# Performance work log

Hardware: AMD Instinct MI355X
Metric: run time of the kernel (lower is better)

## Reference

```python
import jax, jax.numpy as jnp
import numpy as np

N = 50000      # nodes
E = 1600000    # edges (before self loops)
IN = 128
OUT = 128
H = 4
HD = OUT // H  # head dim = 32


def setup_inputs() -> dict:
    key = jax.random.key(0)
    k1, k2, k3, k4, k5 = jax.random.split(key, 5)
    x = jax.random.normal(k1, (N, IN), dtype=jnp.float32)
    edge_index = jax.random.randint(k2, (2, E), 0, N, dtype=jnp.int64)
    # xavier-uniform-ish scales
    W = jax.random.normal(k3, (OUT, IN), dtype=jnp.float32) * (1.0 / np.sqrt(IN))
    att_src = jax.random.normal(k4, (1, H, HD), dtype=jnp.float32) * 0.1
    att_dst = jax.random.normal(k5, (1, H, HD), dtype=jnp.float32) * 0.1
    return {"x": x, "edge_index": edge_index, "W": W, "att_src": att_src, "att_dst": att_dst}


def reference(x, edge_index, W, att_src, att_dst):
    n = x.shape[0]
    # add self loops (tg.utils.add_self_loops appends [i, i] edges)
    loops = jnp.arange(n, dtype=edge_index.dtype)
    ei = jnp.concatenate([edge_index, jnp.stack([loops, loops])], axis=1)
    src, dst = ei[0], ei[1]

    # linear projection, split into heads: [n, H, HD]
    h = (x @ W.T).reshape(n, H, HD)

    # per-node attention logits per head: [n, H]
    a_src = jnp.sum(h * att_src, axis=-1)
    a_dst = jnp.sum(h * att_dst, axis=-1)

    # per-edge attention score: gather + leaky_relu
    alpha = a_src[src] + a_dst[dst]                      # [Etot, H]
    alpha = jax.nn.leaky_relu(alpha, negative_slope=0.2)

    # segment softmax grouped by destination node (numerically stable)
    m = jax.ops.segment_max(alpha, dst, num_segments=n)  # [n, H]
    e = jnp.exp(alpha - m[dst])
    s = jax.ops.segment_sum(e, dst, num_segments=n)      # [n, H]
    e = e / s[dst]                                       # [Etot, H]

    # weighted scatter-add aggregation; f_additive adds 1 to the weights
    msg = h[src] * (e[:, :, None] + 1.0)                 # [Etot, H, HD]
    out = jax.ops.segment_sum(msg, dst, num_segments=n)  # [n, H, HD]
    return out.reshape(n, -1)
```

## Files before the change

kernel.cpp:

```cpp
#include <hip/hip_runtime.h>

#define N_NODES 50000
#define E_EDGES 1600000
#define ETOT    (E_EDGES + N_NODES)
#define DIN  128
#define DOUT 128
#define NH   4
#define HD   32

typedef unsigned short ushort_t;
typedef unsigned int uint_t;
typedef __attribute__((ext_vector_type(8))) short bfrag;
typedef __attribute__((ext_vector_type(4))) float ffrag;

__device__ __forceinline__ ushort_t f2bf(float f) {
  uint_t u = __float_as_uint(f);
  u += 0x7fffu + ((u >> 16) & 1u);
  return (ushort_t)(u >> 16);
}
__device__ __forceinline__ float bf_lo(uint_t u) {
  return __uint_as_float(u << 16);
}
__device__ __forceinline__ float bf_hi(uint_t u) {
  return __uint_as_float(u & 0xffff0000u);
}

#define BSZ   64
#define NBUCK ((N_NODES + BSZ - 1) / BSZ)
#define CAP   2560
#define EPB_A 4096
#define NBLK_A ((ETOT + EPB_A - 1) / EPB_A)
#define NCHUNK 13

__global__ __launch_bounds__(256, 4) void fused_binA_gemm_kernel(
    const int* __restrict__ ei, int* __restrict__ gcur,
    uint_t* __restrict__ ebuf,
    const float* __restrict__ x, const float* __restrict__ W,
    const float* __restrict__ att_src, const float* __restrict__ att_dst,
    ushort_t* __restrict__ hb, float* __restrict__ a_src,
    float* __restrict__ a_dst) {
  __shared__ int hist[NBUCK];
  __shared__ int base[NBUCK];
  __shared__ ushort_t Ws[DIN * DOUT];
  const int tid = threadIdx.x;

  if (blockIdx.x < NBLK_A) {
    const int e0 = blockIdx.x * EPB_A;
    const int e1 = min(e0 + EPB_A, ETOT);
    for (int i = tid; i < NBUCK; i += 256) hist[i] = 0;
    __syncthreads();
    for (int e = e0 + tid; e < e1; e += 256) {
      int di = (e < E_EDGES) ? ei[E_EDGES + e] : (e - E_EDGES);
      atomicAdd(&hist[di >> 6], 1);
    }
    __syncthreads();
    for (int i = tid; i < NBUCK; i += 256) {
      int c = hist[i];
      base[i] = (c > 0) ? (i * CAP + atomicAdd(&gcur[i], c)) : 0;
      hist[i] = 0;
    }
    __syncthreads();
    for (int e = e0 + tid; e < e1; e += 256) {
      int si, di;
      if (e < E_EDGES) { si = ei[e]; di = ei[E_EDGES + e]; }
      else             { si = e - E_EDGES; di = si; }
      int b = di >> 6;
      int pos = base[b] + atomicAdd(&hist[b], 1);
      if (pos < (b + 1) * CAP)
        ebuf[pos] = ((uint_t)(di & 63) << 24) | (uint_t)si;
    }
    return;
  }

  const int gb = blockIdx.x - NBLK_A;
  for (int u = tid; u < 2048; u += 256) {
    int row = u >> 4;
    float4 w0 = *(const float4*)&W[u * 8];
    float4 w1 = *(const float4*)&W[u * 8 + 4];
    uint4 pk;
    pk.x = (uint_t)f2bf(w0.x) | ((uint_t)f2bf(w0.y) << 16);
    pk.y = (uint_t)f2bf(w0.z) | ((uint_t)f2bf(w0.w) << 16);
    pk.z = (uint_t)f2bf(w1.x) | ((uint_t)f2bf(w1.y) << 16);
    pk.w = (uint_t)f2bf(w1.z) | ((uint_t)f2bf(w1.w) << 16);
    *(uint4*)&Ws[(u ^ (row & 7)) * 8] = pk;
  }
  __syncthreads();

  const int wv = tid >> 6, l = tid & 63;
  const int lr = l & 15, lg = l >> 4;
  const int nbase = gb * 64 + wv * 16;
  int na = nbase + lr;
  if (na >= N_NODES) na = N_NODES - 1;
  const float* xrow = x + (size_t)na * DIN;

  ffrag acc[8];
#pragma unroll
  for (int oc = 0; oc < 8; oc++) acc[oc] = (ffrag){0.f, 0.f, 0.f, 0.f};

#pragma unroll
  for (int kt = 0; kt < 4; kt++) {
    float4 x0 = *(const float4*)&xrow[kt * 32 + lg * 8];
    float4 x1 = *(const float4*)&xrow[kt * 32 + lg * 8 + 4];
    bfrag a;
    a[0] = (short)f2bf(x0.x); a[1] = (short)f2bf(x0.y);
    a[2] = (short)f2bf(x0.z); a[3] = (short)f2bf(x0.w);
    a[4] = (short)f2bf(x1.x); a[5] = (short)f2bf(x1.y);
    a[6] = (short)f2bf(x1.z); a[7] = (short)f2bf(x1.w);
#pragma unroll
    for (int oc = 0; oc < 8; oc++) {
      const int u = ((oc * 16 + lr) << 4) + kt * 4 + lg;
      const bfrag b = *(const bfrag*)&Ws[(u ^ (lr & 7)) * 8];
      acc[oc] = __builtin_amdgcn_mfma_f32_16x16x32_bf16(a, b, acc[oc], 0, 0, 0);
    }
  }

#pragma unroll
  for (int oc = 0; oc < 8; oc++) {
#pragma unroll
    for (int j = 0; j < 4; j++) {
      int n = nbase + lg * 4 + j;
      if (n < N_NODES)
        hb[((size_t)n << 7) + oc * 16 + lr] = f2bf(acc[oc][j]);
    }
  }

  float asv[8], adv[8];
#pragma unroll
  for (int oc = 0; oc < 8; oc++) {
    asv[oc] = att_src[oc * 16 + lr];
    adv[oc] = att_dst[oc * 16 + lr];
  }
#pragma unroll
  for (int j = 0; j < 4; j++) {
    float ps[4] = {0.f, 0.f, 0.f, 0.f};
    float pd[4] = {0.f, 0.f, 0.f, 0.f};
#pragma unroll
    for (int oc = 0; oc < 8; oc++) {
      ps[oc >> 1] = fmaf(acc[oc][j], asv[oc], ps[oc >> 1]);
      pd[oc >> 1] = fmaf(acc[oc][j], adv[oc], pd[oc >> 1]);
    }
#pragma unroll
    for (int off = 1; off < 16; off <<= 1) {
#pragma unroll
      for (int hd = 0; hd < 4; hd++) {
        ps[hd] += __shfl_xor(ps[hd], off);
        pd[hd] += __shfl_xor(pd[hd], off);
      }
    }
    int n = nbase + lg * 4 + j;
    if (n < N_NODES && lr < 4) {
      float vs = lr == 0 ? ps[0] : lr == 1 ? ps[1] : lr == 2 ? ps[2] : ps[3];
      float vd = lr == 0 ? pd[0] : lr == 1 ? pd[1] : lr == 2 ? pd[2] : pd[3];
      a_src[n * NH + lr] = vs;
      a_dst[n * NH + lr] = vd;
    }
  }
}

__global__ __launch_bounds__(256) void binB_kernel(
    const uint_t* __restrict__ ebuf, const int* __restrict__ gcur,
    int* __restrict__ rs, int* __restrict__ re, int* __restrict__ col) {
  __shared__ int cnt[BSZ * NCHUNK];
  __shared__ int roff[BSZ * NCHUNK];
  const int b = blockIdx.x;
  const int tid = threadIdx.x;
  const int n0 = b << 6;
  const int nn = min(BSZ, N_NODES - n0);
  const int s0 = b * CAP;
  const int s1 = s0 + min(gcur[b], CAP);
  for (int k = tid; k < BSZ * NCHUNK; k += 256) cnt[k] = 0;
  __syncthreads();
  for (int i = s0 + tid; i < s1; i += 256) {
    uint_t p = ebuf[i];
    int key = (int)(p >> 24) * NCHUNK + (int)((p & 0xFFFFFFu) >> 12);
    atomicAdd(&cnt[key], 1);
  }
  __syncthreads();
  if (tid < BSZ) {
    int pref[NCHUNK];
    int tot = 0;
#pragma unroll
    for (int k = 0; k < NCHUNK; k++) { pref[k] = tot; tot += cnt[tid * NCHUNK + k]; }
    int xx = tot;
#pragma unroll
    for (int off = 1; off < 64; off <<= 1) {
      int y = __shfl_up(xx, off, 64);
      if (tid >= off) xx += y;
    }
    const int nodebase = xx - tot;
#pragma unroll
    for (int k = 0; k < NCHUNK; k++) roff[tid * NCHUNK + k] = nodebase + pref[k];
    if (tid < nn) {
      rs[n0 + tid] = s0 + nodebase;
      re[n0 + tid] = s0 + nodebase + tot;
    }
  }
  __syncthreads();
  for (int k = tid; k < BSZ * NCHUNK; k += 256) cnt[k] = 0;
  __syncthreads();
  for (int i = s0 + tid; i < s1; i += 256) {
    uint_t p = ebuf[i];
    int si = (int)(p & 0xFFFFFFu);
    int key = (int)(p >> 24) * NCHUNK + (si >> 12);
    int pos = atomicAdd(&cnt[key], 1);
    int q = s0 + roff[key] + pos;
    if (q >= 0 && q < NBUCK * CAP) col[q] = si;
  }
}

#define NPB 16
#define CH  16

__global__ __launch_bounds__(256, 8) void agg_kernel(
    const int* __restrict__ col, const int* __restrict__ rs,
    const int* __restrict__ re, const ushort_t* __restrict__ hb,
    const float* __restrict__ a_src, const float* __restrict__ a_dst,
    float* __restrict__ out) {
  __shared__ float w_lds[NPB][CH][NH];
  __shared__ int   si_lds[NPB][CH];
  const int tid  = threadIdx.x;
  const int slot = tid >> 4;
  const int t    = tid & 15;
  const int node = blockIdx.x * NPB + slot;
  const int start = rs[node];
  const int deg   = re[node] - start;
  const float4 ad = *(const float4*)(a_dst + (size_t)node * NH);

  const int head = t >> 2;
  const int c8 = t << 3;
  const ushort_t* hc = hb + c8;
  float s = 0.f;
  float a0 = 0.f, a1 = 0.f, a2 = 0.f, a3 = 0.f;
  float a4 = 0.f, a5 = 0.f, a6 = 0.f, a7 = 0.f;
  float b0 = 0.f, b1 = 0.f, b2 = 0.f, b3 = 0.f;
  float b4 = 0.f, b5 = 0.f, b6 = 0.f, b7 = 0.f;

  for (int base_e = 0; base_e < deg; base_e += CH) {
    int nch = deg - base_e;
    if (nch > CH) nch = CH;
    if (t < nch) {
      int si = col[start + base_e + t];
      si = si < N_NODES ? si : 0;
      si_lds[slot][t] = si;
      float4 as = *(const float4*)(a_src + (size_t)si * NH);
      float v0 = as.x + ad.x; v0 = v0 > 0.f ? v0 : 0.2f * v0;
      float v1 = as.y + ad.y; v1 = v1 > 0.f ? v1 : 0.2f * v1;
      float v2 = as.z + ad.z; v2 = v2 > 0.f ? v2 : 0.2f * v2;
      float v3 = as.w + ad.w; v3 = v3 > 0.f ? v3 : 0.2f * v3;
      w_lds[slot][t][0] = __expf(v0);
      w_lds[slot][t][1] = __expf(v1);
      w_lds[slot][t][2] = __expf(v2);
      w_lds[slot][t][3] = __expf(v3);
    }
    __builtin_amdgcn_fence(__ATOMIC_ACQ_REL, "wavefront");
#pragma unroll 2
    for (int j = 0; j < nch; j++) {
      int si = si_lds[slot][j];
      float e = w_lds[slot][j][head];
      s += e;
      const uint4 hv = *(const uint4*)(hc + ((size_t)si << 7));
      float h0 = bf_lo(hv.x), h1 = bf_hi(hv.x);
      float h2 = bf_lo(hv.y), h3 = bf_hi(hv.y);
      float h4 = bf_lo(hv.z), h5 = bf_hi(hv.z);
      float h6 = bf_lo(hv.w), h7 = bf_hi(hv.w);
      a0 = fmaf(h0, e, a0); b0 += h0;
      a1 = fmaf(h1, e, a1); b1 += h1;
      a2 = fmaf(h2, e, a2); b2 += h2;
      a3 = fmaf(h3, e, a3); b3 += h3;
      a4 = fmaf(h4, e, a4); b4 += h4;
      a5 = fmaf(h5, e, a5); b5 += h5;
      a6 = fmaf(h6, e, a6); b6 += h6;
      a7 = fmaf(h7, e, a7); b7 += h7;
    }
    __builtin_amdgcn_fence(__ATOMIC_ACQ_REL, "wavefront");
  }
  const float inv = 1.0f / s;
  float* op = out + ((size_t)node << 7) + c8;
  *(float4*)(op)     = make_float4(fmaf(a0, inv, b0), fmaf(a1, inv, b1),
                                   fmaf(a2, inv, b2), fmaf(a3, inv, b3));
  *(float4*)(op + 4) = make_float4(fmaf(a4, inv, b4), fmaf(a5, inv, b5),
                                   fmaf(a6, inv, b6), fmaf(a7, inv, b7));
}

extern "C" void kernel_launch(void* const* d_in, const int* in_sizes, int n_in,
                              void* d_out, int out_size, void* d_ws, size_t ws_size,
                              hipStream_t stream) {
  const float* x       = (const float*)d_in[0];
  const int*   ei      = (const int*)d_in[1];
  const float* W       = (const float*)d_in[2];
  const float* att_src = (const float*)d_in[3];
  const float* att_dst = (const float*)d_in[4];
  float* out = (float*)d_out;

  ushort_t* hb = (ushort_t*)d_ws;
  float* a_src = (float*)(hb + (size_t)N_NODES * DOUT);
  float* a_dst = a_src + (size_t)N_NODES * NH;
  int* gcur    = (int*)(a_dst + (size_t)N_NODES * NH);
  int* rs      = gcur + NBUCK;
  int* re      = rs + N_NODES;
  int* col     = re + N_NODES;
  uint_t* ebuf = (uint_t*)(col + (size_t)NBUCK * CAP);

  hipMemsetAsync(gcur, 0, (size_t)NBUCK * sizeof(int), stream);

  const int gemm_blocks = (N_NODES + 63) / 64;
  fused_binA_gemm_kernel<<<NBLK_A + gemm_blocks, 256, 0, stream>>>(
      ei, gcur, ebuf, x, W, att_src, att_dst, hb, a_src, a_dst);
  binB_kernel<<<NBUCK, 256, 0, stream>>>(ebuf, gcur, rs, re, col);
  agg_kernel<<<N_NODES / NPB, 256, 0, stream>>>(col, rs, re, hb, a_src, a_dst, out);
}
```

Measured before the change: 105.3 us.

## Load W fragments directly from global memory instead of staging in LDS

The GEMM blocks no longer convert and stage the full weight matrix into shared memory. Each lane now reads its B fragment straight from global W (expected to hit L2 cache) and converts it to bf16 in registers. This drops the 32KB LDS array and a block-wide barrier, which can raise occupancy for both the binning and GEMM blocks. The cost is redundant global loads and bf16 conversions of W in every block. Edges per binning block are also doubled, which halves the binning block count and the per-block histogram setup.

```diff
diff --git a/kernel.cpp b/kernel.cpp
--- a/kernel.cpp
+++ b/kernel.cpp
@@ -24,11 +24,19 @@
 __device__ __forceinline__ float bf_hi(uint_t u) {
   return __uint_as_float(u & 0xffff0000u);
 }
+__device__ __forceinline__ bfrag cvt_frag(float4 v0, float4 v1) {
+  bfrag a;
+  a[0] = (short)f2bf(v0.x); a[1] = (short)f2bf(v0.y);
+  a[2] = (short)f2bf(v0.z); a[3] = (short)f2bf(v0.w);
+  a[4] = (short)f2bf(v1.x); a[5] = (short)f2bf(v1.y);
+  a[6] = (short)f2bf(v1.z); a[7] = (short)f2bf(v1.w);
+  return a;
+}
 
 #define BSZ   64
 #define NBUCK ((N_NODES + BSZ - 1) / BSZ)
 #define CAP   2560
-#define EPB_A 4096
+#define EPB_A 8192
 #define NBLK_A ((ETOT + EPB_A - 1) / EPB_A)
 #define NCHUNK 13
 
@@ -41,7 +49,6 @@
     float* __restrict__ a_dst) {
   __shared__ int hist[NBUCK];
   __shared__ int base[NBUCK];
-  __shared__ ushort_t Ws[DIN * DOUT];
   const int tid = threadIdx.x;
 
   if (blockIdx.x < NBLK_A) {
@@ -73,25 +80,13 @@
   }
 
   const int gb = blockIdx.x - NBLK_A;
-  for (int u = tid; u < 2048; u += 256) {
-    int row = u >> 4;
-    float4 w0 = *(const float4*)&W[u * 8];
-    float4 w1 = *(const float4*)&W[u * 8 + 4];
-    uint4 pk;
-    pk.x = (uint_t)f2bf(w0.x) | ((uint_t)f2bf(w0.y) << 16);
-    pk.y = (uint_t)f2bf(w0.z) | ((uint_t)f2bf(w0.w) << 16);
-    pk.z = (uint_t)f2bf(w1.x) | ((uint_t)f2bf(w1.y) << 16);
-    pk.w = (uint_t)f2bf(w1.z) | ((uint_t)f2bf(w1.w) << 16);
-    *(uint4*)&Ws[(u ^ (row & 7)) * 8] = pk;
-  }
-  __syncthreads();
-
   const int wv = tid >> 6, l = tid & 63;
   const int lr = l & 15, lg = l >> 4;
   const int nbase = gb * 64 + wv * 16;
   int na = nbase + lr;
   if (na >= N_NODES) na = N_NODES - 1;
   const float* xrow = x + (size_t)na * DIN;
+  const float* wbase = W + (size_t)lr * DIN;
 
   ffrag acc[8];
 #pragma unroll
@@ -99,17 +94,16 @@
 
 #pragma unroll
   for (int kt = 0; kt < 4; kt++) {
-    float4 x0 = *(const float4*)&xrow[kt * 32 + lg * 8];
-    float4 x1 = *(const float4*)&xrow[kt * 32 + lg * 8 + 4];
-    bfrag a;
-    a[0] = (short)f2bf(x0.x); a[1] = (short)f2bf(x0.y);
-    a[2] = (short)f2bf(x0.z); a[3] = (short)f2bf(x0.w);
-    a[4] = (short)f2bf(x1.x); a[5] = (short)f2bf(x1.y);
-    a[6] = (short)f2bf(x1.z); a[7] = (short)f2bf(x1.w);
+    const int co = kt * 32 + lg * 8;
+    const float4 x0 = *(const float4*)&xrow[co];
+    const float4 x1 = *(const float4*)&xrow[co + 4];
+    const bfrag a = cvt_frag(x0, x1);
 #pragma unroll
     for (int oc = 0; oc < 8; oc++) {
-      const int u = ((oc * 16 + lr) << 4) + kt * 4 + lg;
-      const bfrag b = *(const bfrag*)&Ws[(u ^ (lr & 7)) * 8];
+      const float* wrow = wbase + (size_t)(oc * 16) * DIN + co;
+      const float4 w0 = *(const float4*)wrow;
+      const float4 w1 = *(const float4*)(wrow + 4);
+      const bfrag b = cvt_frag(w0, w1);
       acc[oc] = __builtin_amdgcn_mfma_f32_16x16x32_bf16(a, b, acc[oc], 0, 0, 0);
     }
   }
```

Result: slower. 123.5 us (+17.3%).
